# Kernel optimization log

Hardware: AMD Instinct MI355X
Metric: run time of the kernel (lower is better)

The kernel has to match this reference:

```python
import jax, jax.numpy as jnp
import numpy as np

B, S, H, D = 2, 4096, 32, 128  # batch, seq_len, num_heads, key_size
BLOCK = 128                     # block_size (S must be divisible)


def setup_inputs() -> dict:
    key = jax.random.key(0)
    kq, kk, kv = jax.random.split(key, 3)
    q = jax.random.normal(kq, (B, S, H * D), dtype=jnp.float32)
    k = jax.random.normal(kk, (B, S, H * D), dtype=jnp.float32)
    v = jax.random.normal(kv, (B, S, H * D), dtype=jnp.float32)
    return {"q": q, "k": k, "v": v}


def reference(q, k, v):
    batch, seq_len, _ = q.shape
    nb = seq_len // BLOCK  # num_blocks
    # reshape to [B, nb, block, H, D]
    qb = q.reshape(batch, nb, BLOCK, H, D)
    kb = k.reshape(batch, nb, BLOCK, H, D)
    vb = v.reshape(batch, nb, BLOCK, H, D)
    scale = np.float32(1.0 / np.sqrt(D))
    # Faithful to original einsum '...hd,...kd->...hk': contraction is over d
    # with (nb, block) as batch dims, so attention runs over the HEAD axis (g).
    logits = jnp.einsum("bnshd,bnsgd->bnshg", qb, kb) * scale  # [B,nb,block,H,H]
    w = jax.nn.softmax(logits, axis=-1)
    out = jnp.einsum("bnshg,bnsgd->bnshd", w, vb)  # [B,nb,block,H,D]
    return out.reshape(batch, seq_len, H * D)
```

## Files before the change

### kernel.cpp

```cpp
#include <hip/hip_runtime.h>


typedef __bf16 bf16x8 __attribute__((ext_vector_type(8)));
typedef __bf16 bf16x2 __attribute__((ext_vector_type(2)));
typedef float  f32x4  __attribute__((ext_vector_type(4)));

static constexpr float kScale = 0.08838834764831845f;
static constexpr int kTPW = 4;

typedef const __attribute__((address_space(1))) unsigned int* gas_ptr;
typedef __attribute__((address_space(3))) unsigned int* las_ptr;

__device__ inline bf16x8 to_bf16x8(f32x4 a, f32x4 b) {
  bf16x8 f;
  f[0] = (__bf16)a[0]; f[1] = (__bf16)a[1];
  f[2] = (__bf16)a[2]; f[3] = (__bf16)a[3];
  f[4] = (__bf16)b[0]; f[5] = (__bf16)b[1];
  f[6] = (__bf16)b[2]; f[7] = (__bf16)b[3];
  return f;
}

__global__ __launch_bounds__(64) void attn_headwise(
    const float* __restrict__ q, const float* __restrict__ k,
    const float* __restrict__ v, float* __restrict__ out, int ntok) {
  const int lane = threadIdx.x;
  const int lr   = lane & 15;
  const int G    = lane >> 4;
  const long base = (long)blockIdx.x * kTPW;

  __shared__ __align__(16) float        vbuf[2][32 * 128];
  __shared__ __align__(16) unsigned int pbuf[32 * 20];

  f32x4 kraw[4][2][2], qraw[4][2][2];

  auto clampTok = [&](long t) { return t < (long)ntok ? t : (long)ntok - 1; };

  auto issueQK = [&](long t) {
    const float* kt = k + t * 4096;
    const float* qt = q + t * 4096;
    #pragma unroll
    for (int kk = 0; kk < 4; ++kk)
      #pragma unroll
      for (int tt = 0; tt < 2; ++tt) {
        const float* pk = kt + (16 * tt + lr) * 128 + 32 * kk + 8 * G;
        kraw[kk][tt][0] = *(const f32x4*)pk;
        kraw[kk][tt][1] = *(const f32x4*)(pk + 4);
        const float* pq = qt + (16 * tt + lr) * 128 + 32 * kk + 8 * G;
        qraw[kk][tt][0] = *(const f32x4*)pq;
        qraw[kk][tt][1] = *(const f32x4*)(pq + 4);
      }
  };
  auto issueV = [&](long t, int buf) {
    const float* vsrc = v + t * 4096 + lane * 4;
    float*       vdst = vbuf[buf];
    #pragma unroll
    for (int i = 0; i < 16; ++i)
      __builtin_amdgcn_global_load_lds((gas_ptr)(vsrc + i * 256),
                                       (las_ptr)(vdst + i * 256), 16, 0, 0);
  };

  issueQK(clampTok(base));
  issueV(clampTok(base), 0);

  #pragma unroll
  for (int it = 0; it < kTPW; ++it) {
    const long tok = clampTok(base + it);
    float* ot = out + tok * 4096;

    f32x4 acc[2][2];
    acc[0][0] = 0.f; acc[0][1] = 0.f; acc[1][0] = 0.f; acc[1][1] = 0.f;
    #pragma unroll
    for (int kk = 0; kk < 4; ++kk) {
      bf16x8 kf[2], qf[2];
      #pragma unroll
      for (int tt = 0; tt < 2; ++tt) {
        kf[tt] = to_bf16x8(kraw[kk][tt][0], kraw[kk][tt][1]);
        qf[tt] = to_bf16x8(qraw[kk][tt][0], qraw[kk][tt][1]);
      }
      #pragma unroll
      for (int gi = 0; gi < 2; ++gi)
        #pragma unroll
        for (int hj = 0; hj < 2; ++hj)
          acc[gi][hj] = __builtin_amdgcn_mfma_f32_16x16x32_bf16(
              kf[gi], qf[hj], acc[gi][hj], 0, 0, 0);
    }

    if (it + 1 < kTPW) {
      issueQK(clampTok(base + it + 1));
      issueV(clampTok(base + it + 1), (it + 1) & 1);
    }
    __builtin_amdgcn_sched_barrier(0);

    #pragma unroll
    for (int hj = 0; hj < 2; ++hj) {
      float m = acc[0][hj][0];
      #pragma unroll
      for (int gi = 0; gi < 2; ++gi)
        #pragma unroll
        for (int r = 0; r < 4; ++r) m = fmaxf(m, acc[gi][hj][r]);
      m = fmaxf(m, __shfl_xor(m, 16, 64));
      m = fmaxf(m, __shfl_xor(m, 32, 64));

      float pv[2][4];
      float s = 0.f;
      #pragma unroll
      for (int gi = 0; gi < 2; ++gi)
        #pragma unroll
        for (int r = 0; r < 4; ++r) {
          float e = __expf((acc[gi][hj][r] - m) * kScale);
          pv[gi][r] = e;
          s += e;
        }
      s += __shfl_xor(s, 16, 64);
      s += __shfl_xor(s, 32, 64);
      float inv = 1.0f / s;

      #pragma unroll
      for (int gi = 0; gi < 2; ++gi)
        #pragma unroll
        for (int mp = 0; mp < 2; ++mp) {
          bf16x2 t2;
          t2[0] = (__bf16)(pv[gi][2 * mp]     * inv);
          t2[1] = (__bf16)(pv[gi][2 * mp + 1] * inv);
          pbuf[(16 * hj + lr) * 20 + 8 * gi + 2 * G + mp] =
              __builtin_bit_cast(unsigned int, t2);
        }
    }
    bf16x8 pf[2];
    #pragma unroll
    for (int ht = 0; ht < 2; ++ht)
      pf[ht] = *(const bf16x8*)&pbuf[(16 * ht + lr) * 20 + 4 * G];

    if (it + 1 < kTPW) {
      asm volatile("s_waitcnt vmcnt(48)" ::: "memory");
    } else {
      asm volatile("s_waitcnt vmcnt(0)" ::: "memory");
    }
    __builtin_amdgcn_sched_barrier(0);

    const float* vl = vbuf[it & 1];
    f32x4 zero = 0.f;
    #pragma unroll
    for (int dt = 0; dt < 8; ++dt) {
      bf16x8 vf;
      #pragma unroll
      for (int e = 0; e < 8; ++e)
        vf[e] = (__bf16)vl[(8 * G + e) * 128 + 16 * dt + lr];
      f32x4 o0 = __builtin_amdgcn_mfma_f32_16x16x32_bf16(vf, pf[0], zero, 0, 0, 0);
      f32x4 o1 = __builtin_amdgcn_mfma_f32_16x16x32_bf16(vf, pf[1], zero, 0, 0, 0);
      *(f32x4*)&ot[lr * 128 + 16 * dt + 4 * G]        = o0;
      *(f32x4*)&ot[(16 + lr) * 128 + 16 * dt + 4 * G] = o1;
    }
  }
}

extern "C" void kernel_launch(void* const* d_in, const int* in_sizes, int n_in,
                              void* d_out, int out_size, void* d_ws, size_t ws_size,
                              hipStream_t stream) {
  const float* q = (const float*)d_in[0];
  const float* k = (const float*)d_in[1];
  const float* v = (const float*)d_in[2];
  float* out = (float*)d_out;
  int ntok = in_sizes[0] / 4096;
  int grid = (ntok + kTPW - 1) / kTPW;
  hipLaunchKernelGGL(attn_headwise, dim3(grid), dim3(64), 0, stream,
                     q, k, v, out, ntok);
}
```

Before: 117.2 us.

## Stage Q/K/V through swizzled LDS via direct global-to-LDS loads

Q and K are now loaded straight into LDS with global_load_lds instead of into registers, using an XOR-swizzled layout so fragment reads avoid bank conflicts, and V uses the same swizzle. Each operand has a single LDS buffer that is refilled for the next token as soon as the current token's fragments have been read. Tokens per wave go from 4 to 8 and the loop is no longer unrolled. This frees the large raw-register arrays, which could raise occupancy, but it adds LDS traffic and leaves less room to overlap loads with compute.

```diff
diff --git a/kernel.cpp b/kernel.cpp
--- a/kernel.cpp
+++ b/kernel.cpp
@@ -6,10 +6,16 @@
 typedef float  f32x4  __attribute__((ext_vector_type(4)));
 
 static constexpr float kScale = 0.08838834764831845f;
-static constexpr int kTPW = 4;
+static constexpr int kTPW = 8;
 
 typedef const __attribute__((address_space(1))) unsigned int* gas_ptr;
 typedef __attribute__((address_space(3))) unsigned int* las_ptr;
+
+#define WAITV16() asm volatile("s_waitcnt vmcnt(16)" ::: "memory")
+#define WAITV32() asm volatile("s_waitcnt vmcnt(32)" ::: "memory")
+#define WAITV0()  asm volatile("s_waitcnt vmcnt(0)"  ::: "memory")
+#define WAITL0()  asm volatile("s_waitcnt lgkmcnt(0)" ::: "memory")
+#define SBAR()    __builtin_amdgcn_sched_barrier(0)
 
 __device__ inline bf16x8 to_bf16x8(f32x4 a, f32x4 b) {
   bf16x8 f;
@@ -27,69 +33,73 @@
   const int lr   = lane & 15;
   const int G    = lane >> 4;
   const long base = (long)blockIdx.x * kTPW;
+  if (base >= ntok) return;
 
-  __shared__ __align__(16) float        vbuf[2][32 * 128];
+  __shared__ __align__(16) float        qls[32 * 128];
+  __shared__ __align__(16) float        kls[32 * 128];
+  __shared__ __align__(16) float        vls[32 * 128];
   __shared__ __align__(16) unsigned int pbuf[32 * 20];
 
-  f32x4 kraw[4][2][2], qraw[4][2][2];
+  int soff[4];
+  {
+    const int b = lane >> 5;
+    #pragma unroll
+    for (int j = 0; j < 4; ++j)
+      soff[j] = b * 128 + 4 * ((lane & 31) ^ (((2 * j) & 7) + b));
+  }
+  auto stage = [&](const float* tokbase, float* dst) {
+    #pragma unroll
+    for (int i = 0; i < 16; ++i)
+      __builtin_amdgcn_global_load_lds((gas_ptr)(tokbase + i * 256 + soff[i & 3]),
+                                       (las_ptr)(dst + i * 256), 16, 0, 0);
+  };
+  auto frag = [&](const float* ls, int kk, int tt) -> bf16x8 {
+    const int row = 16 * tt + lr;
+    const int c0  = 8 * kk + 2 * G;
+    f32x4 a = *(const f32x4*)&ls[row * 128 + 4 * ((c0)     ^ (row & 7))];
+    f32x4 b = *(const f32x4*)&ls[row * 128 + 4 * ((c0 + 1) ^ (row & 7))];
+    return to_bf16x8(a, b);
+  };
 
-  auto clampTok = [&](long t) { return t < (long)ntok ? t : (long)ntok - 1; };
+  stage(k + base * 4096, kls);
+  stage(q + base * 4096, qls);
+  stage(v + base * 4096, vls);
 
-  auto issueQK = [&](long t) {
-    const float* kt = k + t * 4096;
-    const float* qt = q + t * 4096;
+  #pragma unroll 1
+  for (int it = 0; it < kTPW; ++it) {
+    const long tok = base + it;
+    float* ot = out + tok * 4096;
+
+    if (it == 0) { WAITV16(); } else { WAITV32(); }
+    SBAR();
+
+    bf16x8 kf[4][2], qf[4][2];
     #pragma unroll
     for (int kk = 0; kk < 4; ++kk)
       #pragma unroll
       for (int tt = 0; tt < 2; ++tt) {
-        const float* pk = kt + (16 * tt + lr) * 128 + 32 * kk + 8 * G;
-        kraw[kk][tt][0] = *(const f32x4*)pk;
-        kraw[kk][tt][1] = *(const f32x4*)(pk + 4);
-        const float* pq = qt + (16 * tt + lr) * 128 + 32 * kk + 8 * G;
-        qraw[kk][tt][0] = *(const f32x4*)pq;
-        qraw[kk][tt][1] = *(const f32x4*)(pq + 4);
+        kf[kk][tt] = frag(kls, kk, tt);
+        qf[kk][tt] = frag(qls, kk, tt);
       }
-  };
-  auto issueV = [&](long t, int buf) {
-    const float* vsrc = v + t * 4096 + lane * 4;
-    float*       vdst = vbuf[buf];
-    #pragma unroll
-    for (int i = 0; i < 16; ++i)
-      __builtin_amdgcn_global_load_lds((gas_ptr)(vsrc + i * 256),
-                                       (las_ptr)(vdst + i * 256), 16, 0, 0);
-  };
+    WAITL0();
+    SBAR();
 
-  issueQK(clampTok(base));
-  issueV(clampTok(base), 0);
-
-  #pragma unroll
-  for (int it = 0; it < kTPW; ++it) {
-    const long tok = clampTok(base + it);
-    float* ot = out + tok * 4096;
+    if (it + 1 < kTPW) {
+      stage(k + (tok + 1) * 4096, kls);
+      stage(q + (tok + 1) * 4096, qls);
+    }
+    SBAR();
 
     f32x4 acc[2][2];
     acc[0][0] = 0.f; acc[0][1] = 0.f; acc[1][0] = 0.f; acc[1][1] = 0.f;
     #pragma unroll
-    for (int kk = 0; kk < 4; ++kk) {
-      bf16x8 kf[2], qf[2];
-      #pragma unroll
-      for (int tt = 0; tt < 2; ++tt) {
-        kf[tt] = to_bf16x8(kraw[kk][tt][0], kraw[kk][tt][1]);
-        qf[tt] = to_bf16x8(qraw[kk][tt][0], qraw[kk][tt][1]);
-      }
+    for (int kk = 0; kk < 4; ++kk)
       #pragma unroll
       for (int gi = 0; gi < 2; ++gi)
         #pragma unroll
         for (int hj = 0; hj < 2; ++hj)
           acc[gi][hj] = __builtin_amdgcn_mfma_f32_16x16x32_bf16(
-              kf[gi], qf[hj], acc[gi][hj], 0, 0, 0);
-    }
-
-    if (it + 1 < kTPW) {
-      issueQK(clampTok(base + it + 1));
-      issueV(clampTok(base + it + 1), (it + 1) & 1);
-    }
-    __builtin_amdgcn_sched_barrier(0);
+              kf[kk][gi], qf[kk][hj], acc[gi][hj], 0, 0, 0);
 
     #pragma unroll
     for (int hj = 0; hj < 2; ++hj) {
@@ -131,26 +141,28 @@
     for (int ht = 0; ht < 2; ++ht)
       pf[ht] = *(const bf16x8*)&pbuf[(16 * ht + lr) * 20 + 4 * G];
 
-    if (it + 1 < kTPW) {
-      asm volatile("s_waitcnt vmcnt(48)" ::: "memory");
-    } else {
-      asm volatile("s_waitcnt vmcnt(0)" ::: "memory");
-    }
-    __builtin_amdgcn_sched_barrier(0);
+    if (it + 1 == kTPW) { WAITV0(); } else { WAITV32(); }
+    SBAR();
 
-    const float* vl = vbuf[it & 1];
     f32x4 zero = 0.f;
     #pragma unroll
     for (int dt = 0; dt < 8; ++dt) {
       bf16x8 vf;
       #pragma unroll
-      for (int e = 0; e < 8; ++e)
-        vf[e] = (__bf16)vl[(8 * G + e) * 128 + 16 * dt + lr];
+      for (int e = 0; e < 8; ++e) {
+        const int row = 8 * G + e;
+        vf[e] = (__bf16)vls[row * 128 +
+                            4 * ((4 * dt + (lr >> 2)) ^ (row & 7)) + (lr & 3)];
+      }
       f32x4 o0 = __builtin_amdgcn_mfma_f32_16x16x32_bf16(vf, pf[0], zero, 0, 0, 0);
       f32x4 o1 = __builtin_amdgcn_mfma_f32_16x16x32_bf16(vf, pf[1], zero, 0, 0, 0);
       *(f32x4*)&ot[lr * 128 + 16 * dt + 4 * G]        = o0;
       *(f32x4*)&ot[(16 + lr) * 128 + 16 * dt + 4 * G] = o1;
     }
+    WAITL0();
+    SBAR();
+
+    if (it + 1 < kTPW) stage(v + (tok + 1) * 4096, vls);
   }
 }
 
```

New measurement: 123.4 us. 5.3% more time.
